# Optimization experiments

Hardware: AMD Instinct MI355X
Metric: run time of the kernel (lower is better)

The kernel has to match this reference:

```python
import jax, jax.numpy as jnp
import numpy as np
from jax import lax

B, T, L, OUT, SP, E, H = 128, 300, 28, 28, 7, 20, 256
W = T - L + 1          # 273 sliding windows
W_OUT = W - OUT        # 245 training windows
F_IN = L + 1 + E       # 49 rnn input features


def _lstm_dilated(x, d, Wih, Whh, b):
    # x: [T0, B, F]; dilation d realized by phase-stacking time into batch (zalando DRNN scheme)
    T0, Bn, F = x.shape
    pad = (-T0) % d
    if pad:
        x = jnp.concatenate([x, jnp.zeros((pad, Bn, F), x.dtype)], axis=0)
    Tn = x.shape[0] // d
    xd = x.reshape(Tn, d * Bn, F)  # element [k, j*Bn:(j+1)*Bn] == x[k*d+j]
    Hh = Whh.shape[1]

    def step(carry, xt):
        h, c = carry
        z = xt @ Wih.T + h @ Whh.T + b
        i, f, g, o = jnp.split(z, 4, axis=-1)  # torch LSTM gate order i,f,g,o
        c = jax.nn.sigmoid(f) * c + jax.nn.sigmoid(i) * jnp.tanh(g)
        h = jax.nn.sigmoid(o) * jnp.tanh(c)
        return (h, c), h

    h0 = jnp.zeros((d * Bn, Hh), x.dtype)
    _, hs = lax.scan(step, (h0, h0), xd)
    return hs.reshape(Tn * d, Bn, Hh)[:T0]


def _forward(train_dataset, val_dataset, alpha_raw, gamma_raw, init_seas,
             input_categories, my_param,
             Wih1, Whh1, b1, Wih2, Whh2, b2, Wih3, Whh3, b3, Wih4, Whh4, b4,
             linear_W, linear_b, score_W, score_b):
    x = train_dataset
    a = jax.nn.sigmoid(alpha_raw)   # [B]
    g = jax.nn.sigmoid(gamma_raw)   # [B]
    S0 = jnp.exp(init_seas)         # [B,7] = seasonalities[0..6]
    s7 = S0[:, 0]                   # seasonalities[7] = exp(init[:,0])
    level0 = x[:, 0] / S0[:, 0]
    buf0 = jnp.concatenate([S0[:, 1:], s7[:, None]], axis=1)  # S[1..7], shift register

    def es_step(carry, xt):
        level, buf = carry
        s = buf[:, 0]
        lvl = a * (xt / s) + (1.0 - a) * level
        s_new = g * (xt / lvl) + (1.0 - g) * s
        buf = jnp.concatenate([buf[:, 1:], s_new[:, None]], axis=1)
        return (lvl, buf), (lvl, s_new)

    _, (lvls, s_news) = lax.scan(es_step, (level0, buf0), x[:, 1:].T)
    levels = jnp.concatenate([level0[None], lvls], axis=0).T        # [B,T]
    S_full = jnp.concatenate([S0, s7[:, None], s_news.T], axis=1)   # [B,T+7]
    # extension: cat(S_full, S_full[:, T : T-7+28])  -> [B, T+28]
    S_ext = jnp.concatenate([S_full, S_full[:, T:T - SP + OUT]], axis=1)

    # input windows (vectorized over all W window positions)
    widx = jnp.arange(W)[:, None] + jnp.arange(L)[None, :]          # [W,L]
    lvl_w = levels[:, L - 1 + jnp.arange(W)]                        # [B,W]
    norm_in = x[:, widx] / S_ext[:, widx] / lvl_w[:, :, None]       # [B,W,L]
    cats = jnp.broadcast_to(input_categories[:, None, :], (B, W, E))
    cat_in = jnp.concatenate([norm_in, cats], axis=2)[jnp.arange(B) % 10]  # original j%10 row pick
    mp = jnp.broadcast_to(my_param.reshape(1, 1, 1), (B, W, 1))
    window_input = jnp.transpose(jnp.concatenate([cat_in, mp], axis=2), (1, 0, 2))  # [W,B,F_IN]

    # output windows
    oidx = (L + jnp.arange(W_OUT))[:, None] + jnp.arange(OUT)[None, :]  # [W_OUT,OUT]
    lvl_o = levels[:, L - 1 + jnp.arange(W_OUT)]                        # [B,W_OUT]
    window_output = jnp.transpose(x[:, oidx] / S_ext[:, oidx] / lvl_o[:, :, None], (1, 0, 2))

    # residual dilated LSTM stack: block1 dilations (1,2); block2 dilations (2,6) + residual
    h1 = _lstm_dilated(window_input, 1, Wih1, Whh1, b1)
    h1 = _lstm_dilated(h1, 2, Wih2, Whh2, b2)
    h2 = _lstm_dilated(h1, 2, Wih3, Whh3, b3)
    h2 = _lstm_dilated(h2, 6, Wih4, Whh4, b4) + h1
    h = jnp.tanh(h2 @ linear_W.T + linear_b)
    rnn_out = h @ score_W.T + score_b                                   # [W,B,OUT]

    # LSTM stack is causal, so running on window_input[:-OUT] equals slicing the full run
    prediction_values = rnn_out[:-OUT]
    actual_values = window_output
    holdout = rnn_out[-1] * S_ext[:, -OUT:] * levels[:, -1:]
    holdout_prediction = holdout * (holdout > 0).astype(holdout.dtype)
    hav = val_dataset
    hav_norm = hav / S_ext[:, -OUT:] / levels[:, -1:]
    return (prediction_values, actual_values, holdout_prediction, rnn_out, hav, hav_norm)


def setup_inputs() -> dict:
    key = jax.random.key(0)
    ks = jax.random.split(key, 24)
    s = float(1.0 / np.sqrt(H))
    u = lambda k, shape: jax.random.uniform(k, shape, jnp.float32, -s, s)
    inp = {
        "train_dataset": jax.random.uniform(ks[0], (B, T), jnp.float32) * 2.0 + 0.5,  # positive sales
        "val_dataset": jax.random.uniform(ks[1], (B, OUT), jnp.float32) * 2.0 + 0.5,
        "alpha_raw": jnp.full((B,), 0.5, jnp.float32),
        "gamma_raw": jnp.full((B,), 0.5, jnp.float32),
        "init_seas": jnp.full((B, SP), 0.5, jnp.float32),
        "input_categories": jnp.full((B, E), 0.001, jnp.float32) + 0.01 * jax.random.normal(ks[2], (B, E), jnp.float32),
        "my_param": jnp.full((1,), 0.001, jnp.float32),
        "Wih1": u(ks[3], (4 * H, F_IN)), "Whh1": u(ks[4], (4 * H, H)), "b1": u(ks[5], (4 * H,)),
        "Wih2": u(ks[6], (4 * H, H)), "Whh2": u(ks[7], (4 * H, H)), "b2": u(ks[8], (4 * H,)),
        "Wih3": u(ks[9], (4 * H, H)), "Whh3": u(ks[10], (4 * H, H)), "b3": u(ks[11], (4 * H,)),
        "Wih4": u(ks[12], (4 * H, H)), "Whh4": u(ks[13], (4 * H, H)), "b4": u(ks[14], (4 * H,)),
        "linear_W": u(ks[15], (H, H)), "linear_b": u(ks[16], (H,)),
        "score_W": u(ks[17], (OUT, H)), "score_b": u(ks[18], (OUT,)),
    }
    return inp


def reference(train_dataset, val_dataset, alpha_raw, gamma_raw, init_seas,
              input_categories, my_param,
              Wih1, Whh1, b1, Wih2, Whh2, b2, Wih3, Whh3, b3, Wih4, Whh4, b4,
              linear_W, linear_b, score_W, score_b):
    return _forward(train_dataset, val_dataset, alpha_raw, gamma_raw, init_seas,
                    input_categories, my_param,
                    Wih1, Whh1, b1, Wih2, Whh2, b2, Wih3, Whh3, b3, Wih4, Whh4, b4,
                    linear_W, linear_b, score_W, score_b)
```

## Files before the change

### kernel.cpp

```cpp
#include <hip/hip_runtime.h>

typedef unsigned short u16;
typedef unsigned int   u32;

static __device__ __forceinline__ float sigf (float x){ return 1.0f/(1.0f+__expf(-x)); }
static __device__ __forceinline__ float tanh_(float x){ return 2.0f/(1.0f+__expf(-2.0f*x)) - 1.0f; }

#define NM 2730
#define N_O0 878080
#define N_O3 978432

static __device__ __forceinline__ int dot4(u32 a, u32 b, int acc){
#if __has_builtin(__builtin_amdgcn_sdot4)
  return __builtin_amdgcn_sdot4((int)a, (int)b, acc, false);
#else
  int s = acc;
  #pragma unroll
  for(int i=0;i<4;i++){
    int av = (int)((signed char)((a >> (8*i)) & 0xffu));
    int bv = (int)((signed char)((b >> (8*i)) & 0xffu));
    s += av*bv;
  }
  return s;
#endif
}

__global__ __launch_bounds__(256) void k_prep(
    const float* __restrict__ x,     float* __restrict__ xT,
    const float* __restrict__ wi0,   float* __restrict__ wT0,
    const float* __restrict__ wi1,   float* __restrict__ wT1,
    const float* __restrict__ wi2,   float* __restrict__ wT2,
    const float* __restrict__ wi3,   float* __restrict__ wT3,
    const float* __restrict__ lw,    float* __restrict__ lwT,
    const float* __restrict__ sw,    float* __restrict__ swT,
    const float* __restrict__ h0, const float* __restrict__ h1,
    const float* __restrict__ h2, const float* __restrict__ h3,
    float* __restrict__ zsc){
  int i = blockIdx.x*256 + threadIdx.x;
  if(i < 38400){
    int t = i >> 7, b = i & 127;
    xT[i] = x[b*300 + t];
    return;
  }
  i -= 38400;
  if(i < 50176){ int c=i/1024, r=i-c*1024; wT0[i] = wi0[r*49 + c];  return; }
  i -= 50176;
  if(i < 262144){ int c=i>>10, r=i&1023; wT1[i] = wi1[r*256 + c];   return; }
  i -= 262144;
  if(i < 262144){ int c=i>>10, r=i&1023; wT2[i] = wi2[r*256 + c];   return; }
  i -= 262144;
  if(i < 262144){ int c=i>>10, r=i&1023; wT3[i] = wi3[r*256 + c];   return; }
  i -= 262144;
  if(i < 65536){ int c=i>>8, r=i&255; lwT[i] = lw[r*256 + c];       return; }
  i -= 65536;
  if(i < 7168){ int c=i/28, r=i-c*28; swT[i] = sw[r*256 + c];       return; }
  i -= 7168;
  if(i < 4096){
    int l = i >> 10, r = i & 1023;
    const float* W = (l==0)?h0:(l==1)?h1:(l==2)?h2:h3;
    const float4* p = (const float4*)(W + (size_t)r*256);
    float m = 0.f;
    #pragma unroll 8
    for(int q=0;q<64;q++){
      float4 v = p[q];
      m = fmaxf(m, fmaxf(fmaxf(fabsf(v.x),fabsf(v.y)), fmaxf(fabsf(v.z),fabsf(v.w))));
    }
    zsc[i] = fmaxf(m, 1e-20f) * (1.0f/16129.0f);
  }
}

__global__ __launch_bounds__(256) void k_packes(
    const float* __restrict__ h0, const float* __restrict__ h1,
    const float* __restrict__ h2, const float* __restrict__ h3,
    const float* __restrict__ zsc, u32* __restrict__ W8,
    const float* __restrict__ xT, const float* __restrict__ alpha,
    const float* __restrict__ gamma, const float* __restrict__ iseas,
    float* __restrict__ ST, float* __restrict__ lvlT){
  if(blockIdx.x < 1024){
    int i = blockIdx.x*256 + threadIdx.x;
    int l = i >> 16;
    int uidx = i & 65535;
    int dw = uidx & 3;
    int kg = (uidx >> 2) & 127;
    int q  = (uidx >> 9) & 3;
    int rr = (uidx >> 11) & 7;
    int js = uidx >> 14;
    int row = rr*128 + kg;
    int k0  = js*64 + q*16 + dw*4;
    const float* W = (l==0)?h0:(l==1)?h1:(l==2)?h2:h3;
    float inv = 1.0f / (zsc[l*1024 + row] * 127.0f);
    u32 out = 0;
    #pragma unroll
    for(int b=0;b<4;b++){
      float v = W[(size_t)row*256 + k0 + b];
      int q8 = max(-127, min(127, __float2int_rn(v * inv)));
      out |= ((u32)(q8 & 0xff)) << (8*b);
    }
    W8[i] = out;
    return;
  }
  int b = threadIdx.x;
  if(b >= 128) return;
  float a = sigf(alpha[b]);
  float g = sigf(gamma[b]);
  float S0[7];
  #pragma unroll
  for(int i=0;i<7;i++){ S0[i] = __expf(iseas[b*7+i]); ST[i*128+b] = S0[i]; }
  ST[7*128+b] = S0[0];
  float q0=S0[1],q1=S0[2],q2=S0[3],q3=S0[4],q4=S0[5],q5=S0[6],q6=S0[0];
  float lvl = xT[b]/S0[0];
  lvlT[b] = lvl;
  for(int t=1;t<300;t++){
    float xt = xT[t*128+b];
    float s  = q0;
    lvl = a*(xt/s) + (1.0f-a)*lvl;
    float sn = g*(xt/lvl) + (1.0f-g)*s;
    q0=q1;q1=q2;q2=q3;q3=q4;q4=q5;q5=q6;q6=sn;
    lvlT[t*128+b]   = lvl;
    ST[(t+7)*128+b] = sn;
  }
}

__global__ __launch_bounds__(256) void k_gemm1(
    const float* __restrict__ xT, const float* __restrict__ ST,
    const float* __restrict__ lvlT, const float* __restrict__ cats,
    const float* __restrict__ mp,
    const float* __restrict__ WT,
    const float* __restrict__ bias,
    float* __restrict__ Z){
  __shared__ float Xs[8][52];
  const int tid = threadIdx.x;
  const int m0 = blockIdx.x*8;
  for(int idx=tid; idx<8*49; idx+=256){
    int p = idx/49, f = idx - p*49;
    int m = m0+p;
    float v = 0.f;
    if(m < NM){
      int tt = m/10, jj = m - (m/10)*10;
      if(f < 28){
        int c = tt + f;
        v = xT[c*128 + jj] / ST[c*128 + jj] / lvlT[(tt+27)*128 + jj];
      } else if(f < 48){
        v = cats[jj*20 + (f-28)];
      } else {
        v = mp[0];
      }
    }
    Xs[p][f] = v;
  }
  __syncthreads();
  float acc0[8], acc1[8], acc2[8], acc3[8];
  {
    float b0 = bias[tid];
    float b1 = bias[tid+256];
    float b2 = bias[tid+512];
    float b3 = bias[tid+768];
    #pragma unroll
    for(int p=0;p<8;p++){ acc0[p]=b0; acc1[p]=b1; acc2[p]=b2; acc3[p]=b3; }
  }
  #pragma unroll 7
  for(int f=0; f<49; f++){
    float w0 = WT[f*1024 + tid      ];
    float w1 = WT[f*1024 + tid+256  ];
    float w2 = WT[f*1024 + tid+512  ];
    float w3 = WT[f*1024 + tid+768  ];
    #pragma unroll
    for(int p=0;p<8;p++){
      float xv = Xs[p][f];
      acc0[p] += w0*xv; acc1[p] += w1*xv; acc2[p] += w2*xv; acc3[p] += w3*xv;
    }
  }
  for(int p=0;p<8;p++){
    int m = m0+p;
    if(m < NM){
      float* zb = Z + m*1024 + tid;
      zb[0]=acc0[p]; zb[256]=acc1[p]; zb[512]=acc2[p]; zb[768]=acc3[p];
    }
  }
}

__global__ __launch_bounds__(256) void k_gemm(const float* __restrict__ X,
                                              const float* __restrict__ WT,
                                              const float* __restrict__ bias,
                                              float* __restrict__ Z){
  __shared__ float Xs[8][256];
  const int tid = threadIdx.x;
  const int m0 = blockIdx.x*8;
  for(int p=0;p<8;p++){
    int m = m0+p;
    Xs[p][tid] = (m < NM) ? X[m*256+tid] : 0.0f;
  }
  __syncthreads();
  float acc0[8], acc1[8], acc2[8], acc3[8];
  {
    float b0 = bias[tid];
    float b1 = bias[tid+256];
    float b2 = bias[tid+512];
    float b3 = bias[tid+768];
    #pragma unroll
    for(int p=0;p<8;p++){ acc0[p]=b0; acc1[p]=b1; acc2[p]=b2; acc3[p]=b3; }
  }
  #pragma unroll 4
  for(int f=0; f<256; f++){
    float w0 = WT[f*1024 + tid      ];
    float w1 = WT[f*1024 + tid+256  ];
    float w2 = WT[f*1024 + tid+512  ];
    float w3 = WT[f*1024 + tid+768  ];
    #pragma unroll
    for(int p=0;p<8;p++){
      float xv = Xs[p][f];
      acc0[p] += w0*xv; acc1[p] += w1*xv; acc2[p] += w2*xv; acc3[p] += w3*xv;
    }
  }
  for(int p=0;p<8;p++){
    int m = m0+p;
    if(m < NM){
      float* zb = Z + m*1024 + tid;
      zb[0]=acc0[p]; zb[256]=acc1[p]; zb[512]=acc2[p]; zb[768]=acc3[p];
    }
  }
}

__global__ __launch_bounds__(512, 2) void k_scan8(
    const float* __restrict__ Z,
    const u32* __restrict__ W8,
    const float* __restrict__ zsc,
    float* __restrict__ Y,
    const float* __restrict__ RES,
    int d){
  __shared__ __align__(16) u32 h8[64];
  __shared__ int   zp[4][1024];
  __shared__ float sc[1024];
  const int tid = threadIdx.x;
  const int chain = blockIdx.x;
  const int j = chain % 10;
  const int r = chain / 10;
  const int ns = (273 - r + d - 1)/d;
  const int kg = tid & 127;
  const int js = tid >> 7;
  const uint4* Wb = (const uint4*)W8 + (size_t)js*4096 + kg;
  const uint4* hq = (const uint4*)h8 + js*4;

  uint4 wreg[32];
  #pragma unroll
  for(int q=0;q<4;q++){
    #pragma unroll
    for(int rr=0;rr<8;rr++){
      wreg[q*8+rr] = Wb[rr*512 + q*128];
    }
  }

  for(int i=tid;i<1024;i+=512) sc[i] = zsc[i];
  if(tid < 64) h8[tid] = 0u;
  float cst = 0.0f;
  __syncthreads();

  int t = r;
  for(int s=0; s<ns; s++, t+=d){
    const size_t row = (size_t)(t*10 + j);
    float zv0=0.f, zv1=0.f, zv2=0.f, zv3=0.f, rv=0.f;
    if(tid < 256){
      const float* zb = Z + row*1024;
      zv0 = zb[tid]; zv1 = zb[tid+256]; zv2 = zb[tid+512]; zv3 = zb[tid+768];
      if(RES) rv = RES[row*256 + tid];
    }
    int a0=0,a1=0,a2=0,a3=0,a4=0,a5=0,a6=0,a7=0;
    #pragma unroll
    for(int q=0;q<4;q++){
      uint4 h4 = hq[q];
      #pragma unroll
      for(int rr=0;rr<8;rr++){
        uint4 w = wreg[q*8+rr];
        int* ap = (rr==0)?&a0:(rr==1)?&a1:(rr==2)?&a2:(rr==3)?&a3:
                  (rr==4)?&a4:(rr==5)?&a5:(rr==6)?&a6:&a7;
        int acc = *ap;
        acc = dot4(w.x, h4.x, acc);
        acc = dot4(w.y, h4.y, acc);
        acc = dot4(w.z, h4.z, acc);
        acc = dot4(w.w, h4.w, acc);
        *ap = acc;
      }
    }
    zp[js][       kg] = a0;
    zp[js][128  + kg] = a1;
    zp[js][256  + kg] = a2;
    zp[js][384  + kg] = a3;
    zp[js][512  + kg] = a4;
    zp[js][640  + kg] = a5;
    zp[js][768  + kg] = a6;
    zp[js][896  + kg] = a7;
    __syncthreads();
    if(tid < 256){
      const int u = tid;
      int si = zp[0][u]     + zp[1][u]     + zp[2][u]     + zp[3][u];
      int sf = zp[0][u+256] + zp[1][u+256] + zp[2][u+256] + zp[3][u+256];
      int sg = zp[0][u+512] + zp[1][u+512] + zp[2][u+512] + zp[3][u+512];
      int so = zp[0][u+768] + zp[1][u+768] + zp[2][u+768] + zp[3][u+768];
      float zi = zv0 + sc[u]     * (float)si;
      float zf = zv1 + sc[u+256] * (float)sf;
      float zg = zv2 + sc[u+512] * (float)sg;
      float zo = zv3 + sc[u+768] * (float)so;
      float c  = sigf(zf)*cst + sigf(zi)*tanh_(zg);
      float h  = sigf(zo)*tanh_(c);
      cst = c;
      int hqi = __float2int_rn(h * 127.0f);
      hqi = max(-127, min(127, hqi));
      ((signed char*)h8)[u] = (signed char)hqi;
      Y[row*256 + u] = h + rv;
    }
    asm volatile("s_waitcnt lgkmcnt(0)\n\ts_barrier" ::: "memory");
  }
}

__global__ __launch_bounds__(256) void k_headout(const float* __restrict__ Y4,
    const float* __restrict__ LWT,
    const float* __restrict__ lb,
    const float* __restrict__ SWT,
    const float* __restrict__ sb,
    const float* __restrict__ ST, const float* __restrict__ lvlT,
    const float* __restrict__ xT, const float* __restrict__ val,
    float* __restrict__ out){
  __shared__ float v [8][256];
  __shared__ float h2[8][256];
  const int tid = threadIdx.x;
  if(blockIdx.x >= 342){
    int i = (blockIdx.x - 342)*256 + tid;
    if(i < N_O0){
      int o = i % 28;
      int b = (i/28) % 128;
      int t = i/(28*128);
      int c = 28 + t + o;
      out[878080 + i] = xT[c*128+b] / ST[c*128+b] / lvlT[(27+t)*128+b];
    } else {
      i -= N_O0;
      if(i < 3584){
        int b = i/28, o = i%28;
        int col = (o < 21) ? (286+o) : (279+o);
        float Sm = ST[col*128 + b];
        float lv = lvlT[299*128 + b];
        out[2738176 + i] = val[i];
        out[2741760 + i] = val[i] / Sm / lv;
      }
    }
    return;
  }
  const int m0 = blockIdx.x*8;
  for(int p=0;p<8;p++){
    int m = m0+p;
    v[p][tid] = (m<NM) ? Y4[m*256+tid] : 0.0f;
  }
  __syncthreads();
  float acc[8];
  float bz = lb[tid];
  #pragma unroll
  for(int p=0;p<8;p++) acc[p]=bz;
  #pragma unroll 4
  for(int f=0; f<256; f++){
    float w = LWT[f*256+tid];
    #pragma unroll
    for(int p=0;p<8;p++) acc[p] += w * v[p][f];
  }
  #pragma unroll
  for(int p=0;p<8;p++) h2[p][tid] = tanh_(acc[p]);
  __syncthreads();
  if(tid < 224){
    int o = tid % 28, p = tid / 28;
    int m = m0 + p;
    if(m < NM){
      float a = sb[o];
      for(int f=0; f<256; f++) a += SWT[f*28+o] * h2[p][f];
      int t = m / 10, j = m - t*10;
      float* o0 = out;
      float* o3 = out + 1759744;
      for(int b=j; b<128; b+=10){
        size_t idx = (size_t)t*3584 + b*28 + o;
        o3[idx] = a;
        if(t < 245) o0[idx] = a;
      }
      if(t == 272){
        int col = (o < 21) ? (286+o) : (279+o);
        float* o2 = out + 1756160;
        for(int b=j; b<128; b+=10){
          float hv = a * ST[col*128 + b] * lvlT[299*128 + b];
          o2[b*28 + o] = (hv > 0.0f) ? hv : 0.0f;
        }
      }
    }
  }
}

extern "C" void kernel_launch(void* const* d_in, const int* in_sizes, int n_in,
                              void* d_out, int out_size, void* d_ws, size_t ws_size,
                              hipStream_t stream){
  (void)in_sizes; (void)n_in; (void)out_size; (void)ws_size;
  const float* x     = (const float*)d_in[0];
  const float* val   = (const float*)d_in[1];
  const float* alpha = (const float*)d_in[2];
  const float* gamma = (const float*)d_in[3];
  const float* iseas = (const float*)d_in[4];
  const float* cats  = (const float*)d_in[5];
  const float* mp    = (const float*)d_in[6];
  const float* Wih[4]  = {(const float*)d_in[7],  (const float*)d_in[10], (const float*)d_in[13], (const float*)d_in[16]};
  const float* Whh[4]  = {(const float*)d_in[8],  (const float*)d_in[11], (const float*)d_in[14], (const float*)d_in[17]};
  const float* bias[4] = {(const float*)d_in[9],  (const float*)d_in[12], (const float*)d_in[15], (const float*)d_in[18]};
  const float* linW  = (const float*)d_in[19];
  const float* linb  = (const float*)d_in[20];
  const float* scW   = (const float*)d_in[21];
  const float* scb   = (const float*)d_in[22];

  float* Fw   = (float*)d_ws;
  float* ST   = Fw;
  float* lvlT = ST   + 39296;
  float* xT   = lvlT + 38400;
  float* xz   = xT   + 38400;
  float* yA   = xz   + 2795520;
  float* yB   = yA   + 698880;
  float* wihT[4];
  wihT[0] = yB + 698880;
  wihT[1] = wihT[0] + 50176;
  wihT[2] = wihT[1] + 262144;
  wihT[3] = wihT[2] + 262144;
  float* linWT = wihT[3] + 262144;
  float* scT   = linWT + 65536;
  float* zsc   = scT   + 7168;
  u32*   W8all = (u32*)(zsc + 4096);

  k_prep<<<3718, 256, 0, stream>>>(x, xT,
      Wih[0], wihT[0], Wih[1], wihT[1], Wih[2], wihT[2], Wih[3], wihT[3],
      linW, linWT, scW, scT,
      Whh[0], Whh[1], Whh[2], Whh[3], zsc);

  k_packes<<<1025, 256, 0, stream>>>(Whh[0], Whh[1], Whh[2], Whh[3], zsc, W8all,
                                     xT, alpha, gamma, iseas, ST, lvlT);

  const int    dlt[4]    = {1, 2, 2, 6};
  const int    chains[4] = {10, 20, 20, 60};
  const float* Xin[4]    = {nullptr, yA, yB, yA};
  float*       Yout[4]   = {yA, yB, yA, yA};
  for(int l=0;l<4;l++){
    if(l == 0)
      k_gemm1<<<(NM+7)/8, 256, 0, stream>>>(xT, ST, lvlT, cats, mp,
                                            wihT[0], bias[0], xz);
    else
      k_gemm<<<(NM+7)/8, 256, 0, stream>>>(Xin[l], wihT[l], bias[l], xz);
    k_scan8<<<chains[l], 512, 0, stream>>>(xz, W8all + l*65536, zsc + l*1024,
                                           Yout[l],
                                           (l==3) ? yB : (const float*)nullptr, dlt[l]);
  }

  k_headout<<<342 + (N_O0 + 3584 + 255)/256, 256, 0, stream>>>(
      yA, linWT, linb, scT, scb, ST, lvlT, xT, val, (float*)d_out);
}
```

Measured before the change: 999.3 us.

## Split recurrent int8 matvec across 1024 threads per scan block

Doubles the scan kernel's block size to 1024 threads. Each thread now holds half as many packed weight registers and computes a shorter dot-product slice, with eight partial-sum slices reduced through shared memory. This shortens the per-step serial dot-product latency on the sequential recurrence. The cost is a larger shared reduction, a wider barrier across more waves, and more shared-memory use per block.

```diff
diff --git a/kernel.cpp b/kernel.cpp
--- a/kernel.cpp
+++ b/kernel.cpp
@@ -221,7 +221,7 @@
   }
 }
 
-__global__ __launch_bounds__(512, 2) void k_scan8(
+__global__ __launch_bounds__(1024) void k_scan8(
     const float* __restrict__ Z,
     const u32* __restrict__ W8,
     const float* __restrict__ zsc,
@@ -229,7 +229,7 @@
     const float* __restrict__ RES,
     int d){
   __shared__ __align__(16) u32 h8[64];
-  __shared__ int   zp[4][1024];
+  __shared__ int   zp[8][1024];
   __shared__ float sc[1024];
   const int tid = threadIdx.x;
   const int chain = blockIdx.x;
@@ -238,19 +238,24 @@
   const int ns = (273 - r + d - 1)/d;
   const int kg = tid & 127;
   const int js = tid >> 7;
-  const uint4* Wb = (const uint4*)W8 + (size_t)js*4096 + kg;
-  const uint4* hq = (const uint4*)h8 + js*4;
-
-  uint4 wreg[32];
-  #pragma unroll
-  for(int q=0;q<4;q++){
-    #pragma unroll
-    for(int rr=0;rr<8;rr++){
-      wreg[q*8+rr] = Wb[rr*512 + q*128];
-    }
-  }
-
-  for(int i=tid;i<1024;i+=512) sc[i] = zsc[i];
+  const uint4* Wb = (const uint4*)W8 + (size_t)(js>>1)*4096 + (js&1)*256 + kg;
+  const uint4* hq = (const uint4*)h8 + js*2;
+
+  uint4 wreg[16];
+  #pragma unroll
+  for(int rr=0;rr<8;rr++){
+    #pragma unroll
+    for(int qq=0;qq<2;qq++){
+      wreg[rr*2+qq] = Wb[rr*512 + qq*128];
+    }
+  }
+  #pragma unroll
+  for(int i=0;i<16;i++){
+    asm volatile("" : "+v"(wreg[i].x), "+v"(wreg[i].y),
+                      "+v"(wreg[i].z), "+v"(wreg[i].w));
+  }
+
+  sc[tid & 1023] = zsc[tid & 1023];
   if(tid < 64) h8[tid] = 0u;
   float cst = 0.0f;
   __syncthreads();
@@ -264,38 +269,34 @@
       zv0 = zb[tid]; zv1 = zb[tid+256]; zv2 = zb[tid+512]; zv3 = zb[tid+768];
       if(RES) rv = RES[row*256 + tid];
     }
-    int a0=0,a1=0,a2=0,a3=0,a4=0,a5=0,a6=0,a7=0;
-    #pragma unroll
-    for(int q=0;q<4;q++){
-      uint4 h4 = hq[q];
-      #pragma unroll
-      for(int rr=0;rr<8;rr++){
-        uint4 w = wreg[q*8+rr];
-        int* ap = (rr==0)?&a0:(rr==1)?&a1:(rr==2)?&a2:(rr==3)?&a3:
-                  (rr==4)?&a4:(rr==5)?&a5:(rr==6)?&a6:&a7;
-        int acc = *ap;
-        acc = dot4(w.x, h4.x, acc);
-        acc = dot4(w.y, h4.y, acc);
-        acc = dot4(w.z, h4.z, acc);
-        acc = dot4(w.w, h4.w, acc);
-        *ap = acc;
-      }
-    }
-    zp[js][       kg] = a0;
-    zp[js][128  + kg] = a1;
-    zp[js][256  + kg] = a2;
-    zp[js][384  + kg] = a3;
-    zp[js][512  + kg] = a4;
-    zp[js][640  + kg] = a5;
-    zp[js][768  + kg] = a6;
-    zp[js][896  + kg] = a7;
+    uint4 h4a = hq[0];
+    uint4 h4b = hq[1];
+    #pragma unroll
+    for(int rr=0;rr<8;rr++){
+      int acc = 0;
+      uint4 w0 = wreg[rr*2+0];
+      acc = dot4(w0.x, h4a.x, acc);
+      acc = dot4(w0.y, h4a.y, acc);
+      acc = dot4(w0.z, h4a.z, acc);
+      acc = dot4(w0.w, h4a.w, acc);
+      uint4 w1 = wreg[rr*2+1];
+      acc = dot4(w1.x, h4b.x, acc);
+      acc = dot4(w1.y, h4b.y, acc);
+      acc = dot4(w1.z, h4b.z, acc);
+      acc = dot4(w1.w, h4b.w, acc);
+      zp[js][rr*128 + kg] = acc;
+    }
     __syncthreads();
     if(tid < 256){
       const int u = tid;
-      int si = zp[0][u]     + zp[1][u]     + zp[2][u]     + zp[3][u];
-      int sf = zp[0][u+256] + zp[1][u+256] + zp[2][u+256] + zp[3][u+256];
-      int sg = zp[0][u+512] + zp[1][u+512] + zp[2][u+512] + zp[3][u+512];
-      int so = zp[0][u+768] + zp[1][u+768] + zp[2][u+768] + zp[3][u+768];
+      int si = zp[0][u]     + zp[1][u]     + zp[2][u]     + zp[3][u]
+             + zp[4][u]     + zp[5][u]     + zp[6][u]     + zp[7][u];
+      int sf = zp[0][u+256] + zp[1][u+256] + zp[2][u+256] + zp[3][u+256]
+             + zp[4][u+256] + zp[5][u+256] + zp[6][u+256] + zp[7][u+256];
+      int sg = zp[0][u+512] + zp[1][u+512] + zp[2][u+512] + zp[3][u+512]
+             + zp[4][u+512] + zp[5][u+512] + zp[6][u+512] + zp[7][u+512];
+      int so = zp[0][u+768] + zp[1][u+768] + zp[2][u+768] + zp[3][u+768]
+             + zp[4][u+768] + zp[5][u+768] + zp[6][u+768] + zp[7][u+768];
       float zi = zv0 + sc[u]     * (float)si;
       float zf = zv1 + sc[u+256] * (float)sf;
       float zg = zv2 + sc[u+512] * (float)sg;
@@ -443,9 +444,9 @@
                                             wihT[0], bias[0], xz);
     else
       k_gemm<<<(NM+7)/8, 256, 0, stream>>>(Xin[l], wihT[l], bias[l], xz);
-    k_scan8<<<chains[l], 512, 0, stream>>>(xz, W8all + l*65536, zsc + l*1024,
-                                           Yout[l],
-                                           (l==3) ? yB : (const float*)nullptr, dlt[l]);
+    k_scan8<<<chains[l], 1024, 0, stream>>>(xz, W8all + l*65536, zsc + l*1024,
+                                            Yout[l],
+                                            (l==3) ? yB : (const float*)nullptr, dlt[l]);
   }
 
   k_headout<<<342 + (N_O0 + 3584 + 255)/256, 256, 0, stream>>>(
```

Measured after the change: 1.053 ms. 1.05x slower.

## Stage recurrent int8 weights in LDS and global instead of registers

Applied to the files above, without the earlier changes.

The recurrent scan kernel no longer holds its int8 recurrent weights in 128 VGPRs per thread. Half of them are copied into a 128KB LDS buffer; the other half is read from global/L2 on every time step. The weight packing layout changes to match. The ES kernel also transposes the input series into a large shared buffer so each thread reads its own series contiguously. The aim is to relieve register pressure and uncoalesced reads. In exchange, both kernels use very large LDS allocations that limit blocks per CU, including the weight-packing blocks. Adding per-step LDS and L2 traffic to the serial scan also risks longer latency.

```diff
diff --git a/kernel.cpp b/kernel.cpp
--- a/kernel.cpp
+++ b/kernel.cpp
@@ -76,17 +76,15 @@
     const float* __restrict__ xT, const float* __restrict__ alpha,
     const float* __restrict__ gamma, const float* __restrict__ iseas,
     float* __restrict__ ST, float* __restrict__ lvlT){
+  __shared__ float xs[128*301];
   if(blockIdx.x < 1024){
     int i = blockIdx.x*256 + threadIdx.x;
     int l = i >> 16;
-    int uidx = i & 65535;
-    int dw = uidx & 3;
-    int kg = (uidx >> 2) & 127;
-    int q  = (uidx >> 9) & 3;
-    int rr = (uidx >> 11) & 7;
-    int js = uidx >> 14;
-    int row = rr*128 + kg;
-    int k0  = js*64 + q*16 + dw*4;
+    int p = i & 65535;
+    int dw  = p & 3;
+    int row = (p >> 2) & 1023;
+    int iw  = p >> 12;
+    int k0  = iw*16 + dw*4;
     const float* W = (l==0)?h0:(l==1)?h1:(l==2)?h2:h3;
     float inv = 1.0f / (zsc[l*1024 + row] * 127.0f);
     u32 out = 0;
@@ -99,6 +97,11 @@
     W8[i] = out;
     return;
   }
+  for(int i=threadIdx.x; i<38400; i+=256){
+    int t = i >> 7, b = i & 127;
+    xs[b*301 + t] = xT[i];
+  }
+  __syncthreads();
   int b = threadIdx.x;
   if(b >= 128) return;
   float a = sigf(alpha[b]);
@@ -108,10 +111,10 @@
   for(int i=0;i<7;i++){ S0[i] = __expf(iseas[b*7+i]); ST[i*128+b] = S0[i]; }
   ST[7*128+b] = S0[0];
   float q0=S0[1],q1=S0[2],q2=S0[3],q3=S0[4],q4=S0[5],q5=S0[6],q6=S0[0];
-  float lvl = xT[b]/S0[0];
+  float lvl = xs[b*301]/S0[0];
   lvlT[b] = lvl;
   for(int t=1;t<300;t++){
-    float xt = xT[t*128+b];
+    float xt = xs[b*301 + t];
     float s  = q0;
     lvl = a*(xt/s) + (1.0f-a)*lvl;
     float sn = g*(xt/lvl) + (1.0f-g)*s;
@@ -221,13 +224,16 @@
   }
 }
 
-__global__ __launch_bounds__(512, 2) void k_scan8(
+__global__ __launch_bounds__(512)
+__attribute__((amdgpu_waves_per_eu(2, 2)))
+void k_scan8(
     const float* __restrict__ Z,
     const u32* __restrict__ W8,
     const float* __restrict__ zsc,
     float* __restrict__ Y,
     const float* __restrict__ RES,
     int d){
+  __shared__ __align__(16) u32 wl[32768];
   __shared__ __align__(16) u32 h8[64];
   __shared__ int   zp[4][1024];
   __shared__ float sc[1024];
@@ -238,18 +244,11 @@
   const int ns = (273 - r + d - 1)/d;
   const int kg = tid & 127;
   const int js = tid >> 7;
-  const uint4* Wb = (const uint4*)W8 + (size_t)js*4096 + kg;
+  const uint4* Wc = (const uint4*)W8;
+  uint4* wl4 = (uint4*)wl;
   const uint4* hq = (const uint4*)h8 + js*4;
 
-  uint4 wreg[32];
-  #pragma unroll
-  for(int q=0;q<4;q++){
-    #pragma unroll
-    for(int rr=0;rr<8;rr++){
-      wreg[q*8+rr] = Wb[rr*512 + q*128];
-    }
-  }
-
+  for(int i=tid;i<8192;i+=512) wl4[i] = Wc[i];
   for(int i=tid;i<1024;i+=512) sc[i] = zsc[i];
   if(tid < 64) h8[tid] = 0u;
   float cst = 0.0f;
@@ -265,20 +264,39 @@
       if(RES) rv = RES[row*256 + tid];
     }
     int a0=0,a1=0,a2=0,a3=0,a4=0,a5=0,a6=0,a7=0;
-    #pragma unroll
-    for(int q=0;q<4;q++){
-      uint4 h4 = hq[q];
+    if(js < 2){
       #pragma unroll
-      for(int rr=0;rr<8;rr++){
-        uint4 w = wreg[q*8+rr];
-        int* ap = (rr==0)?&a0:(rr==1)?&a1:(rr==2)?&a2:(rr==3)?&a3:
-                  (rr==4)?&a4:(rr==5)?&a5:(rr==6)?&a6:&a7;
-        int acc = *ap;
-        acc = dot4(w.x, h4.x, acc);
-        acc = dot4(w.y, h4.y, acc);
-        acc = dot4(w.z, h4.z, acc);
-        acc = dot4(w.w, h4.w, acc);
-        *ap = acc;
+      for(int q=0;q<4;q++){
+        uint4 h4 = hq[q];
+        #pragma unroll
+        for(int rr=0;rr<8;rr++){
+          uint4 w = wl4[(js*4+q)*1024 + rr*128 + kg];
+          int* ap = (rr==0)?&a0:(rr==1)?&a1:(rr==2)?&a2:(rr==3)?&a3:
+                    (rr==4)?&a4:(rr==5)?&a5:(rr==6)?&a6:&a7;
+          int acc = *ap;
+          acc = dot4(w.x, h4.x, acc);
+          acc = dot4(w.y, h4.y, acc);
+          acc = dot4(w.z, h4.z, acc);
+          acc = dot4(w.w, h4.w, acc);
+          *ap = acc;
+        }
+      }
+    } else {
+      #pragma unroll
+      for(int q=0;q<4;q++){
+        uint4 h4 = hq[q];
+        #pragma unroll
+        for(int rr=0;rr<8;rr++){
+          uint4 w = Wc[(js*4+q)*1024 + rr*128 + kg];
+          int* ap = (rr==0)?&a0:(rr==1)?&a1:(rr==2)?&a2:(rr==3)?&a3:
+                    (rr==4)?&a4:(rr==5)?&a5:(rr==6)?&a6:&a7;
+          int acc = *ap;
+          acc = dot4(w.x, h4.x, acc);
+          acc = dot4(w.y, h4.y, acc);
+          acc = dot4(w.z, h4.z, acc);
+          acc = dot4(w.w, h4.w, acc);
+          *ap = acc;
+        }
       }
     }
     zp[js][       kg] = a0;
```

New measurement: 1.381 ms. 1.38x slower.
